# Kernel optimization log

Measured on AMD Instinct MI355X. Metric: run time of the kernel, lower is better.

Reference implementation:

```python
import jax, jax.numpy as jnp
import numpy as np

B, T, D, E, H = 4, 2048, 1024, 8, 4096

def setup_inputs() -> dict:
    key = jax.random.key(0)
    ks = jax.random.split(key, 10)
    s = 0.02
    return {
        "x": jax.random.normal(ks[0], (B, T, D), dtype=jnp.float32),
        "gate_w": jax.random.normal(ks[1], (D, E), dtype=jnp.float32) * s,
        "gate_b": jnp.zeros((E,), dtype=jnp.float32),
        "w1": jax.random.normal(ks[2], (E, D, H), dtype=jnp.float32) * s,
        "b1": jnp.zeros((E, H), dtype=jnp.float32),
        "w2": jax.random.normal(ks[3], (E, D, H), dtype=jnp.float32) * s,
        "b2": jnp.zeros((E, H), dtype=jnp.float32),
        "wp": jax.random.normal(ks[4], (E, H, D), dtype=jnp.float32) * s,
        "bp": jnp.zeros((E, D), dtype=jnp.float32),
        "k": 2,
    }

def reference(x, gate_w, gate_b, w1, b1, w2, b2, wp, bp, k):
    Bq, Tq, Dq = x.shape
    Eq = gate_w.shape[1]
    xf = x.reshape(-1, Dq)                          # [N, D]
    logits = xf @ gate_w + gate_b                   # [N, E]
    topk_scores, topk_idx = jax.lax.top_k(logits, k)  # [N, k]
    gate_probs = jax.nn.softmax(topk_scores, axis=-1)  # [N, k]
    onehot = jax.nn.one_hot(topk_idx, Eq, dtype=x.dtype)  # [N, k, E]
    # per-token per-expert combine weight (0 if expert not in top-k)
    combine = jnp.einsum('nk,nke->ne', gate_probs, onehot)  # [N, E]
    expert_counts = onehot.sum(axis=(0, 1))               # [E]
    out = jnp.zeros_like(xf)
    for e in range(Eq):  # small static loop over experts
        h = jax.nn.silu(xf @ w1[e] + b1[e]) * (xf @ w2[e] + b2[e])  # [N, H]
        y = h @ wp[e] + bp[e]                                       # [N, D]
        out = out + combine[:, e:e + 1] * y
    aux = jnp.sum((expert_counts / expert_counts.sum() - 1.0 / Eq) ** 2)
    return out.reshape(Bq, Tq, Dq), aux
```

## Files before the change

### kernel.cpp

```cpp
#include <hip/hip_runtime.h>
#include <cstdint>
#include <cstddef>

#define N_TOK 8192
#define DIM   1024
#define NEXP  8
#define HID   4096
#define WELEM 4194304ull

typedef __attribute__((ext_vector_type(8))) short short8v;
typedef __attribute__((ext_vector_type(4))) float f32x4;

__device__ __forceinline__ unsigned short f2bf(float f) {
  unsigned u = __builtin_bit_cast(unsigned, f);
  u += 0x7fffu + ((u >> 16) & 1u);
  return (unsigned short)(u >> 16);
}

__device__ __forceinline__ void gload16(const void* g, void* l) {
  __builtin_amdgcn_global_load_lds(
      (const __attribute__((address_space(1))) void*)g,
      (__attribute__((address_space(3))) void*)l, 16, 0, 0);
}

__global__ void convert_x_k(const float* __restrict__ x, unsigned short* __restrict__ xb) {
  size_t i = ((size_t)blockIdx.x * 256 + threadIdx.x) * 8;
  float4 a = *(const float4*)(x + i);
  float4 b = *(const float4*)(x + i + 4);
  short8v v;
  v[0] = (short)f2bf(a.x); v[1] = (short)f2bf(a.y); v[2] = (short)f2bf(a.z); v[3] = (short)f2bf(a.w);
  v[4] = (short)f2bf(b.x); v[5] = (short)f2bf(b.y); v[6] = (short)f2bf(b.z); v[7] = (short)f2bf(b.w);
  *(short8v*)(xb + i) = v;
}

__global__ void gate2_k(const float* __restrict__ x, const float* __restrict__ gw,
                        const float* __restrict__ gb, int* __restrict__ tassign,
                        float2* __restrict__ tprob) {
  int lane = threadIdx.x & 63, wid = threadIdx.x >> 6;
  int t = blockIdx.x * 4 + wid;
  const float* xr = x + (size_t)t * DIM;
  float acc[NEXP];
#pragma unroll
  for (int e = 0; e < NEXP; ++e) acc[e] = 0.f;
#pragma unroll
  for (int j = 0; j < DIM / 256; ++j) {
    int d0 = j * 256 + lane * 4;
    float4 xv = *(const float4*)(xr + d0);
    const float* gp = gw + (size_t)d0 * NEXP;
#pragma unroll
    for (int c = 0; c < 4; ++c) {
      float xs = (c == 0) ? xv.x : (c == 1) ? xv.y : (c == 2) ? xv.z : xv.w;
      float4 g0 = *(const float4*)(gp + c * NEXP);
      float4 g1 = *(const float4*)(gp + c * NEXP + 4);
      acc[0] += xs * g0.x; acc[1] += xs * g0.y; acc[2] += xs * g0.z; acc[3] += xs * g0.w;
      acc[4] += xs * g1.x; acc[5] += xs * g1.y; acc[6] += xs * g1.z; acc[7] += xs * g1.w;
    }
  }
#pragma unroll
  for (int e = 0; e < NEXP; ++e) {
    float v = acc[e];
#pragma unroll
    for (int s = 1; s < 64; s <<= 1) v += __shfl_xor(v, s);
    acc[e] = v;
  }
  if (lane == 0) {
    float lg[NEXP];
#pragma unroll
    for (int e = 0; e < NEXP; ++e) lg[e] = acc[e] + gb[e];
    int i0 = 0;
#pragma unroll
    for (int e = 1; e < NEXP; ++e) if (lg[e] > lg[i0]) i0 = e;
    int i1 = -1;
#pragma unroll
    for (int e = 0; e < NEXP; ++e) if (e != i0 && (i1 < 0 || lg[e] > lg[i1])) i1 = e;
    float ex = expf(lg[i1] - lg[i0]);
    float p0 = 1.f / (1.f + ex);
    float p1 = ex * p0;
    tassign[t] = i0 | (i1 << 8);
    tprob[t] = make_float2(p0, p1);
  }
}

__global__ void route_k(const int* __restrict__ tassign, const float2* __restrict__ tprob,
                        int* __restrict__ rtok, float* __restrict__ rwgt,
                        int* __restrict__ counts, int* __restrict__ ebase) {
  __shared__ int h[NEXP];
  __shared__ int cur[NEXP];
  int tid = threadIdx.x;
  if (tid < NEXP) h[tid] = 0;
  __syncthreads();
  for (int t = tid; t < N_TOK; t += 256) {
    int a = tassign[t];
    atomicAdd(&h[a & 255], 1);
    atomicAdd(&h[(a >> 8) & 255], 1);
  }
  __syncthreads();
  if (tid == 0) {
    int b = 0;
    for (int e = 0; e < NEXP; ++e) { counts[e] = h[e]; ebase[e] = b; cur[e] = b; b += h[e]; }
  }
  __syncthreads();
  for (int t = tid; t < N_TOK; t += 256) {
    int a = tassign[t];
    float2 p = tprob[t];
    int p0 = atomicAdd(&cur[a & 255], 1);
    rtok[p0] = t; rwgt[p0] = p.x;
    int p1 = atomicAdd(&cur[(a >> 8) & 255], 1);
    rtok[p1] = t; rwgt[p1] = p.y;
  }
}

__global__ void aux_k(const int* __restrict__ counts, float* __restrict__ out) {
  if (threadIdx.x == 0) {
    float tot = 0.f, c[NEXP];
    for (int e = 0; e < NEXP; ++e) { c[e] = (float)counts[e]; tot += c[e]; }
    float a = 0.f;
    for (int e = 0; e < NEXP; ++e) { float d = c[e] / tot - 0.125f; a += d * d; }
    out[(size_t)N_TOK * DIM] = a;
  }
}

__global__ void tcvt_k(const float* __restrict__ w1, const float* __restrict__ w2,
                       const float* __restrict__ wp, unsigned short* __restrict__ d1,
                       unsigned short* __restrict__ d2, unsigned short* __restrict__ d3) {
  int tile = blockIdx.x, mat = blockIdx.y;
  size_t eo = (size_t)blockIdx.z * WELEM;
  const float* src; unsigned short* dst; int R, C;
  if (mat == 0)      { src = w1 + eo; dst = d1 + eo; R = DIM; C = HID; }
  else if (mat == 1) { src = w2 + eo; dst = d2 + eo; R = DIM; C = HID; }
  else               { src = wp + eo; dst = d3 + eo; R = HID; C = DIM; }
  int tilesC = C >> 5;
  int tr = (tile / tilesC) << 5;
  int tc = (tile % tilesC) << 5;
  __shared__ float tl[32][33];
  int tx = threadIdx.x & 31, ty = threadIdx.x >> 5;
#pragma unroll
  for (int i = 0; i < 32; i += 8) tl[ty + i][tx] = src[(size_t)(tr + ty + i) * C + tc + tx];
  __syncthreads();
#pragma unroll
  for (int i = 0; i < 32; i += 8) dst[(size_t)(tc + ty + i) * R + tr + tx] = f2bf(tl[tx][ty + i]);
}

template<int DUMMY>
__global__ __launch_bounds__(256, 3) void gemm12m_k(
    const unsigned short* __restrict__ xb,
    const unsigned short* __restrict__ w1b, const unsigned short* __restrict__ w2b,
    const float* __restrict__ b1, const float* __restrict__ b2,
    const int* __restrict__ rtok, const int* __restrict__ counts,
    const int* __restrict__ ebase, const int* __restrict__ gbase,
    unsigned short* __restrict__ Gx, int e0) {
  int f = blockIdx.x + gridDim.x * (blockIdx.y + gridDim.y * blockIdx.z);
  int total = gridDim.x * gridDim.y * gridDim.z;
  int cpx = total >> 3;
  int nf = (f & 7) * cpx + (f >> 3);
  int pe = gridDim.x * gridDim.y;
  int ez = nf / pe;
  int r  = nf - ez * pe;
  int ntb = r >> 5;
  int mt  = r & 31;

  const int e = e0 + ez;
  const int ce = counts[e];
  if (mt * 128 >= ce) return;
  const int rb = ebase[e];
  const int gb_ = gbase[e];
  const unsigned short* w1t = w1b + (size_t)ez * WELEM;
  const unsigned short* w2t = w2b + (size_t)ez * WELEM;
  const float* b1e = b1 + (size_t)e * HID;
  const float* b2e = b2 + (size_t)e * HID;

  __shared__ __attribute__((aligned(16))) unsigned short sA[128 * 64];
  __shared__ __attribute__((aligned(16))) unsigned short sB1[64 * 64];
  __shared__ __attribute__((aligned(16))) unsigned short sB2[64 * 64];

  const int tid = threadIdx.x;
  const int lane = tid & 63, wid = tid >> 6;
  const int wm = wid >> 1, wn = wid & 1;
  const unsigned stg = (unsigned)(wid * 1024);

  const int grow = tid >> 3;
  const int lcol = ((tid & 7) ^ (grow & 7)) << 3;
  int sl0 = mt * 128 + grow;
  int c0 = sl0 < ce ? sl0 : ce - 1;
  int c1 = sl0 + 32 < ce ? sl0 + 32 : ce - 1;
  int c2 = sl0 + 64 < ce ? sl0 + 64 : ce - 1;
  int c3 = sl0 + 96 < ce ? sl0 + 96 : ce - 1;
  const unsigned short* pa0 = xb + (size_t)rtok[rb + c0] * DIM + lcol;
  const unsigned short* pa1 = xb + (size_t)rtok[rb + c1] * DIM + lcol;
  const unsigned short* pa2 = xb + (size_t)rtok[rb + c2] * DIM + lcol;
  const unsigned short* pa3 = xb + (size_t)rtok[rb + c3] * DIM + lcol;
  const unsigned short* pq1 = w1t + (size_t)(ntb * 64 + grow) * DIM + lcol;
  const unsigned short* pq2 = w2t + (size_t)(ntb * 64 + grow) * DIM + lcol;

  f32x4 acc1[4][2] = {};
  f32x4 acc2[4][2] = {};

#pragma unroll 1
  for (int t = 0; t < 16; ++t) {
    const int k0 = t * 64;
    __syncthreads();
    gload16(pa0 + k0, (char*)sA + stg);
    gload16(pa1 + k0, (char*)sA + stg + 4096);
    gload16(pa2 + k0, (char*)sA + stg + 8192);
    gload16(pa3 + k0, (char*)sA + stg + 12288);
    gload16(pq1 + k0, (char*)sB1 + stg);
    gload16(pq1 + k0 + 32 * DIM, (char*)sB1 + stg + 4096);
    gload16(pq2 + k0, (char*)sB2 + stg);
    gload16(pq2 + k0 + 32 * DIM, (char*)sB2 + stg + 4096);
    __syncthreads();
#pragma unroll
    for (int s = 0; s < 2; ++s) {
      short8v af[4], bf1[2], bf2[2];
#pragma unroll
      for (int m = 0; m < 4; ++m) {
        int row = wm * 64 + m * 16 + (lane & 15);
        int p = (s * 4 + (lane >> 4)) ^ (row & 7);
        af[m] = *(const short8v*)((const char*)sA + row * 128 + p * 16);
      }
#pragma unroll
      for (int n = 0; n < 2; ++n) {
        int row = wn * 32 + n * 16 + (lane & 15);
        int p = (s * 4 + (lane >> 4)) ^ (row & 7);
        bf1[n] = *(const short8v*)((const char*)sB1 + row * 128 + p * 16);
        bf2[n] = *(const short8v*)((const char*)sB2 + row * 128 + p * 16);
      }
#pragma unroll
      for (int m = 0; m < 4; ++m)
#pragma unroll
        for (int n = 0; n < 2; ++n) {
          acc1[m][n] = __builtin_amdgcn_mfma_f32_16x16x32_bf16(af[m], bf1[n], acc1[m][n], 0, 0, 0);
          acc2[m][n] = __builtin_amdgcn_mfma_f32_16x16x32_bf16(af[m], bf2[n], acc2[m][n], 0, 0, 0);
        }
    }
  }

#pragma unroll
  for (int n = 0; n < 2; ++n) {
    int col = ntb * 64 + wn * 32 + n * 16 + (lane & 15);
    float bb1 = b1e[col], bb2 = b2e[col];
#pragma unroll
    for (int m = 0; m < 4; ++m) {
      int rbase = mt * 128 + wm * 64 + m * 16 + ((lane >> 4) << 2);
#pragma unroll
      for (int r2 = 0; r2 < 4; ++r2) {
        int slot = rbase + r2;
        if (slot < ce) {
          float h1 = acc1[m][n][r2] + bb1;
          float h2 = acc2[m][n][r2] + bb2;
          float sg = 1.0f / (1.0f + __expf(-h1));
          Gx[(size_t)(gb_ + slot) * HID + col] = f2bf(h1 * sg * h2);
        }
      }
    }
  }
}

#define STG(SD, P0, P1, P2, P3, K0)                                 \
  gload16(P0 + (K0), (char*)SD + stg);                              \
  gload16(P1 + (K0), (char*)SD + stg + 4096);                       \
  gload16(P2 + (K0), (char*)SD + stg + 8192);                       \
  gload16(P3 + (K0), (char*)SD + stg + 12288);

#define CMP()                                                       \
  {                                                                 \
    _Pragma("unroll")                                               \
    for (int s = 0; s < 2; ++s) {                                   \
      short8v af[4], bf[4];                                         \
      _Pragma("unroll")                                             \
      for (int m = 0; m < 4; ++m) {                                 \
        int row = wm * 64 + m * 16 + (lane & 15);                   \
        int p = (s * 4 + (lane >> 4)) ^ (row & 7);                  \
        af[m] = *(const short8v*)((const char*)sA + row * 128 + p * 16); \
      }                                                             \
      _Pragma("unroll")                                             \
      for (int n = 0; n < 4; ++n) {                                 \
        int row = wn * 64 + n * 16 + (lane & 15);                   \
        int p = (s * 4 + (lane >> 4)) ^ (row & 7);                  \
        bf[n] = *(const short8v*)((const char*)sB + row * 128 + p * 16); \
      }                                                             \
      _Pragma("unroll")                                             \
      for (int m = 0; m < 4; ++m)                                   \
        _Pragma("unroll")                                           \
        for (int n = 0; n < 4; ++n)                                 \
          acc[m][n] = __builtin_amdgcn_mfma_f32_16x16x32_bf16(af[m], bf[n], acc[m][n], 0, 0, 0); \
    }                                                               \
  }

#define GEMM_LOOP(NTILE)                                            \
  _Pragma("unroll 1")                                               \
  for (int t = 0; t < (NTILE); ++t) {                               \
    __syncthreads();                                                \
    STG(sA, pa0, pa1, pa2, pa3, t * 64);                            \
    STG(sB, pb0, pb1, pb2, pb3, t * 64);                            \
    __syncthreads();                                                \
    CMP();                                                          \
  }

__global__ __launch_bounds__(256, 4) void gemm3n_k(
    const unsigned short* __restrict__ Gx, const unsigned short* __restrict__ wpb,
    const float* __restrict__ bp, const int* __restrict__ rtok,
    const float* __restrict__ rwgt, const int* __restrict__ counts,
    const int* __restrict__ ebase, const int* __restrict__ gbase,
    float* __restrict__ out, int e0) {
  int f = blockIdx.x + gridDim.x * (blockIdx.y + gridDim.y * blockIdx.z);
  int total = gridDim.x * gridDim.y * gridDim.z;
  int cpx = total >> 3;
  int nf = (f & 7) * cpx + (f >> 3);
  int pe = gridDim.x * gridDim.y;
  int ez = nf / pe;
  int r  = nf - ez * pe;
  int ntb = r >> 5;
  int mt  = r & 31;

  const int e = e0 + ez;
  const int ce = counts[e];
  if (mt * 128 >= ce) return;
  const int rb = ebase[e];
  const int gb_ = gbase[e];
  const unsigned short* wpt = wpb + (size_t)ez * WELEM;
  const float* bpe = bp + (size_t)e * DIM;

  __shared__ __attribute__((aligned(16))) unsigned short sA[128 * 64];
  __shared__ __attribute__((aligned(16))) unsigned short sB[128 * 64];

  const int tid = threadIdx.x;
  const int lane = tid & 63, wid = tid >> 6;
  const int wm = wid >> 1, wn = wid & 1;
  const unsigned stg = (unsigned)(wid * 1024);

  const int grow = tid >> 3;
  const int lcol = ((tid & 7) ^ (grow & 7)) << 3;
  int sl0 = mt * 128 + grow;
  int c0 = sl0 < ce ? sl0 : ce - 1;
  int c1 = sl0 + 32 < ce ? sl0 + 32 : ce - 1;
  int c2 = sl0 + 64 < ce ? sl0 + 64 : ce - 1;
  int c3 = sl0 + 96 < ce ? sl0 + 96 : ce - 1;
  const unsigned short* pa0 = Gx + (size_t)(gb_ + c0) * HID + lcol;
  const unsigned short* pa1 = Gx + (size_t)(gb_ + c1) * HID + lcol;
  const unsigned short* pa2 = Gx + (size_t)(gb_ + c2) * HID + lcol;
  const unsigned short* pa3 = Gx + (size_t)(gb_ + c3) * HID + lcol;
  const unsigned short* pb0 = wpt + (size_t)(ntb * 128 + grow) * HID + lcol;
  const unsigned short* pb1 = pb0 + (size_t)32 * HID;
  const unsigned short* pb2 = pb0 + (size_t)64 * HID;
  const unsigned short* pb3 = pb0 + (size_t)96 * HID;

  f32x4 acc[4][4] = {};
  GEMM_LOOP(64);

#pragma unroll
  for (int n = 0; n < 4; ++n) {
    int col = ntb * 128 + wn * 64 + n * 16 + (lane & 15);
    float bb = bpe[col];
#pragma unroll
    for (int m = 0; m < 4; ++m) {
      int rbase = mt * 128 + wm * 64 + m * 16 + ((lane >> 4) << 2);
#pragma unroll
      for (int r2 = 0; r2 < 4; ++r2) {
        int slot = rbase + r2;
        if (slot < ce) {
          int tok = rtok[rb + slot];
          float w = rwgt[rb + slot];
          atomicAdd(out + (size_t)tok * DIM + col, w * (acc[m][n][r2] + bb));
        }
      }
    }
  }
}

extern "C" void kernel_launch(void* const* d_in, const int* in_sizes, int n_in,
                              void* d_out, int out_size, void* d_ws, size_t ws_size,
                              hipStream_t stream) {
  const float* x  = (const float*)d_in[0];
  const float* gw = (const float*)d_in[1];
  const float* gb = (const float*)d_in[2];
  const float* w1 = (const float*)d_in[3];
  const float* b1 = (const float*)d_in[4];
  const float* w2 = (const float*)d_in[5];
  const float* b2 = (const float*)d_in[6];
  const float* wp = (const float*)d_in[7];
  const float* bp = (const float*)d_in[8];
  float* out = (float*)d_out;

  char* ws = (char*)d_ws;
  const size_t BIG_NEED = 352551008ull;
  bool big = ws_size >= BIG_NEED;

  unsigned short* xb = (unsigned short*)ws;
  unsigned short *Gp, *w1a, *w2a, *wpa;
  int* tassign; float2* tprob; int* rtok; float* rwgt; int* meta;
  if (big) {
    Gp  = (unsigned short*)(ws + 16777216);
    w1a = (unsigned short*)(ws + 150994944);
    w2a = (unsigned short*)(ws + 218103808);
    wpa = (unsigned short*)(ws + 285212672);
    tassign = (int*)(ws + 352321536);
    tprob   = (float2*)(ws + 352354304);
    rtok    = (int*)(ws + 352419840);
    rwgt    = (float*)(ws + 352485376);
    meta    = (int*)(ws + 352550912);
  } else {
    Gp  = (unsigned short*)(ws + 16777216);
    w1a = (unsigned short*)(ws + 83886080);
    w2a = (unsigned short*)(ws + 92274688);
    wpa = (unsigned short*)(ws + 100663296);
    tassign = (int*)(ws + 109051904);
    tprob   = (float2*)(ws + 109084672);
    rtok    = (int*)(ws + 109150208);
    rwgt    = (float*)(ws + 109215744);
    meta    = (int*)(ws + 109281280);
  }
  int* counts = meta;
  int* ebase  = meta + 8;
  int* zbase  = meta + 16;

  hipMemsetAsync(meta, 0, 96, stream);
  hipMemsetAsync(out, 0, (size_t)(N_TOK * DIM + 1) * sizeof(float), stream);

  convert_x_k<<<4096, 256, 0, stream>>>(x, xb);
  gate2_k<<<N_TOK / 4, 256, 0, stream>>>(x, gw, gb, tassign, tprob);
  route_k<<<1, 256, 0, stream>>>(tassign, tprob, rtok, rwgt, counts, ebase);
  aux_k<<<1, 64, 0, stream>>>(counts, out);

  if (big) {
    tcvt_k<<<dim3(4096, 3, NEXP), 256, 0, stream>>>(w1, w2, wp, w1a, w2a, wpa);
    gemm12m_k<0><<<dim3(32, 64, NEXP), 256, 0, stream>>>(
        xb, w1a, w2a, b1, b2, rtok, counts, ebase, ebase, Gp, 0);
    gemm3n_k<<<dim3(32, 8, NEXP), 256, 0, stream>>>(
        Gp, wpa, bp, rtok, rwgt, counts, ebase, ebase, out, 0);
  } else {
    for (int e = 0; e < NEXP; ++e) {
      tcvt_k<<<dim3(4096, 3, 1), 256, 0, stream>>>(
          w1 + (size_t)e * WELEM, w2 + (size_t)e * WELEM, wp + (size_t)e * WELEM,
          w1a, w2a, wpa);
      gemm12m_k<0><<<dim3(32, 64, 1), 256, 0, stream>>>(
          xb, w1a, w2a, b1, b2, rtok, counts, ebase, zbase, Gp, e);
      gemm3n_k<<<dim3(32, 8, 1), 256, 0, stream>>>(
          Gp, wpa, bp, rtok, rwgt, counts, ebase, zbase, out, e);
    }
  }
}
```

Measured before the change: 817.4 us.

## Double-buffer LDS tiles in both expert GEMMs to overlap loads with MFMA

Result: slower. 1.055 ms (+29.1%).

```diff
diff --git a/kernel.cpp b/kernel.cpp
--- a/kernel.cpp
+++ b/kernel.cpp
@@ -22,6 +22,13 @@
       (const __attribute__((address_space(1))) void*)g,
       (__attribute__((address_space(3))) void*)l, 16, 0, 0);
 }
+
+#define VMW8 do { asm volatile("s_waitcnt vmcnt(8)" ::: "memory"); \
+                  __builtin_amdgcn_sched_barrier(0); } while (0)
+#define VMW0 do { asm volatile("s_waitcnt vmcnt(0)" ::: "memory"); \
+                  __builtin_amdgcn_sched_barrier(0); } while (0)
+#define BARR do { __builtin_amdgcn_s_barrier(); \
+                  __builtin_amdgcn_sched_barrier(0); } while (0)
 
 __global__ void convert_x_k(const float* __restrict__ x, unsigned short* __restrict__ xb) {
   size_t i = ((size_t)blockIdx.x * 256 + threadIdx.x) * 8;
@@ -142,7 +149,7 @@
 }
 
 template<int DUMMY>
-__global__ __launch_bounds__(256, 3) void gemm12m_k(
+__global__ __launch_bounds__(256, 2) void gemm12m_k(
     const unsigned short* __restrict__ xb,
     const unsigned short* __restrict__ w1b, const unsigned short* __restrict__ w2b,
     const float* __restrict__ b1, const float* __restrict__ b2,
@@ -169,9 +176,9 @@
   const float* b1e = b1 + (size_t)e * HID;
   const float* b2e = b2 + (size_t)e * HID;
 
-  __shared__ __attribute__((aligned(16))) unsigned short sA[128 * 64];
-  __shared__ __attribute__((aligned(16))) unsigned short sB1[64 * 64];
-  __shared__ __attribute__((aligned(16))) unsigned short sB2[64 * 64];
+  __shared__ __attribute__((aligned(16))) unsigned short sA[2][128 * 64];
+  __shared__ __attribute__((aligned(16))) unsigned short sB1[2][64 * 64];
+  __shared__ __attribute__((aligned(16))) unsigned short sB2[2][64 * 64];
 
   const int tid = threadIdx.x;
   const int lane = tid & 63, wid = tid >> 6;
@@ -195,44 +202,63 @@
   f32x4 acc1[4][2] = {};
   f32x4 acc2[4][2] = {};
 
+#define STAGE12(BUF, K0)                                            \
+  gload16(pa0 + (K0), (char*)sA[BUF] + stg);                        \
+  gload16(pa1 + (K0), (char*)sA[BUF] + stg + 4096);                 \
+  gload16(pa2 + (K0), (char*)sA[BUF] + stg + 8192);                 \
+  gload16(pa3 + (K0), (char*)sA[BUF] + stg + 12288);                \
+  gload16(pq1 + (K0), (char*)sB1[BUF] + stg);                       \
+  gload16(pq1 + (K0) + 32 * DIM, (char*)sB1[BUF] + stg + 4096);     \
+  gload16(pq2 + (K0), (char*)sB2[BUF] + stg);                       \
+  gload16(pq2 + (K0) + 32 * DIM, (char*)sB2[BUF] + stg + 4096);
+
+#define CMP12(BUF)                                                  \
+  {                                                                 \
+    _Pragma("unroll")                                               \
+    for (int s = 0; s < 2; ++s) {                                   \
+      short8v af[4], bf1[2], bf2[2];                                \
+      _Pragma("unroll")                                             \
+      for (int m = 0; m < 4; ++m) {                                 \
+        int row = wm * 64 + m * 16 + (lane & 15);                   \
+        int p = (s * 4 + (lane >> 4)) ^ (row & 7);                  \
+        af[m] = *(const short8v*)((const char*)sA[BUF] + row * 128 + p * 16); \
+      }                                                             \
+      _Pragma("unroll")                                             \
+      for (int n = 0; n < 2; ++n) {                                 \
+        int row = wn * 32 + n * 16 + (lane & 15);                   \
+        int p = (s * 4 + (lane >> 4)) ^ (row & 7);                  \
+        bf1[n] = *(const short8v*)((const char*)sB1[BUF] + row * 128 + p * 16); \
+        bf2[n] = *(const short8v*)((const char*)sB2[BUF] + row * 128 + p * 16); \
+      }                                                             \
+      _Pragma("unroll")                                             \
+      for (int m = 0; m < 4; ++m)                                   \
+        _Pragma("unroll")                                           \
+        for (int n = 0; n < 2; ++n) {                               \
+          acc1[m][n] = __builtin_amdgcn_mfma_f32_16x16x32_bf16(af[m], bf1[n], acc1[m][n], 0, 0, 0); \
+          acc2[m][n] = __builtin_amdgcn_mfma_f32_16x16x32_bf16(af[m], bf2[n], acc2[m][n], 0, 0, 0); \
+        }                                                           \
+    }                                                               \
+  }
+
+  STAGE12(0, 0);
 #pragma unroll 1
-  for (int t = 0; t < 16; ++t) {
-    const int k0 = t * 64;
-    __syncthreads();
-    gload16(pa0 + k0, (char*)sA + stg);
-    gload16(pa1 + k0, (char*)sA + stg + 4096);
-    gload16(pa2 + k0, (char*)sA + stg + 8192);
-    gload16(pa3 + k0, (char*)sA + stg + 12288);
-    gload16(pq1 + k0, (char*)sB1 + stg);
-    gload16(pq1 + k0 + 32 * DIM, (char*)sB1 + stg + 4096);
-    gload16(pq2 + k0, (char*)sB2 + stg);
-    gload16(pq2 + k0 + 32 * DIM, (char*)sB2 + stg + 4096);
-    __syncthreads();
-#pragma unroll
-    for (int s = 0; s < 2; ++s) {
-      short8v af[4], bf1[2], bf2[2];
-#pragma unroll
-      for (int m = 0; m < 4; ++m) {
-        int row = wm * 64 + m * 16 + (lane & 15);
-        int p = (s * 4 + (lane >> 4)) ^ (row & 7);
-        af[m] = *(const short8v*)((const char*)sA + row * 128 + p * 16);
-      }
-#pragma unroll
-      for (int n = 0; n < 2; ++n) {
-        int row = wn * 32 + n * 16 + (lane & 15);
-        int p = (s * 4 + (lane >> 4)) ^ (row & 7);
-        bf1[n] = *(const short8v*)((const char*)sB1 + row * 128 + p * 16);
-        bf2[n] = *(const short8v*)((const char*)sB2 + row * 128 + p * 16);
-      }
-#pragma unroll
-      for (int m = 0; m < 4; ++m)
-#pragma unroll
-        for (int n = 0; n < 2; ++n) {
-          acc1[m][n] = __builtin_amdgcn_mfma_f32_16x16x32_bf16(af[m], bf1[n], acc1[m][n], 0, 0, 0);
-          acc2[m][n] = __builtin_amdgcn_mfma_f32_16x16x32_bf16(af[m], bf2[n], acc2[m][n], 0, 0, 0);
-        }
-    }
-  }
+  for (int i = 0; i < 7; ++i) {
+    STAGE12(1, (2 * i + 1) * 64);
+    VMW8; BARR;
+    CMP12(0);
+    BARR;
+    STAGE12(0, (2 * i + 2) * 64);
+    VMW8; BARR;
+    CMP12(1);
+    BARR;
+  }
+  STAGE12(1, 15 * 64);
+  VMW8; BARR;
+  CMP12(0);
+  VMW0; BARR;
+  CMP12(1);
+#undef STAGE12
+#undef CMP12
 
 #pragma unroll
   for (int n = 0; n < 2; ++n) {
@@ -255,48 +281,7 @@
   }
 }
 
-#define STG(SD, P0, P1, P2, P3, K0)                                 \
-  gload16(P0 + (K0), (char*)SD + stg);                              \
-  gload16(P1 + (K0), (char*)SD + stg + 4096);                       \
-  gload16(P2 + (K0), (char*)SD + stg + 8192);                       \
-  gload16(P3 + (K0), (char*)SD + stg + 12288);
-
-#define CMP()                                                       \
-  {                                                                 \
-    _Pragma("unroll")                                               \
-    for (int s = 0; s < 2; ++s) {                                   \
-      short8v af[4], bf[4];                                         \
-      _Pragma("unroll")                                             \
-      for (int m = 0; m < 4; ++m) {                                 \
-        int row = wm * 64 + m * 16 + (lane & 15);                   \
-        int p = (s * 4 + (lane >> 4)) ^ (row & 7);                  \
-        af[m] = *(const short8v*)((const char*)sA + row * 128 + p * 16); \
-      }                                                             \
-      _Pragma("unroll")                                             \
-      for (int n = 0; n < 4; ++n) {                                 \
-        int row = wn * 64 + n * 16 + (lane & 15);                   \
-        int p = (s * 4 + (lane >> 4)) ^ (row & 7);                  \
-        bf[n] = *(const short8v*)((const char*)sB + row * 128 + p * 16); \
-      }                                                             \
-      _Pragma("unroll")                                             \
-      for (int m = 0; m < 4; ++m)                                   \
-        _Pragma("unroll")                                           \
-        for (int n = 0; n < 4; ++n)                                 \
-          acc[m][n] = __builtin_amdgcn_mfma_f32_16x16x32_bf16(af[m], bf[n], acc[m][n], 0, 0, 0); \
-    }                                                               \
-  }
-
-#define GEMM_LOOP(NTILE)                                            \
-  _Pragma("unroll 1")                                               \
-  for (int t = 0; t < (NTILE); ++t) {                               \
-    __syncthreads();                                                \
-    STG(sA, pa0, pa1, pa2, pa3, t * 64);                            \
-    STG(sB, pb0, pb1, pb2, pb3, t * 64);                            \
-    __syncthreads();                                                \
-    CMP();                                                          \
-  }
-
-__global__ __launch_bounds__(256, 4) void gemm3n_k(
+__global__ __launch_bounds__(256, 2) void gemm3n_k(
     const unsigned short* __restrict__ Gx, const unsigned short* __restrict__ wpb,
     const float* __restrict__ bp, const int* __restrict__ rtok,
     const float* __restrict__ rwgt, const int* __restrict__ counts,
@@ -320,8 +305,8 @@
   const unsigned short* wpt = wpb + (size_t)ez * WELEM;
   const float* bpe = bp + (size_t)e * DIM;
 
-  __shared__ __attribute__((aligned(16))) unsigned short sA[128 * 64];
-  __shared__ __attribute__((aligned(16))) unsigned short sB[128 * 64];
+  __shared__ __attribute__((aligned(16))) unsigned short sA[2][128 * 64];
+  __shared__ __attribute__((aligned(16))) unsigned short sB[2][128 * 64];
 
   const int tid = threadIdx.x;
   const int lane = tid & 63, wid = tid >> 6;
@@ -345,7 +330,61 @@
   const unsigned short* pb3 = pb0 + (size_t)96 * HID;
 
   f32x4 acc[4][4] = {};
-  GEMM_LOOP(64);
+
+#define STG3(BUF, K0)                                               \
+  gload16(pa0 + (K0), (char*)sA[BUF] + stg);                        \
+  gload16(pa1 + (K0), (char*)sA[BUF] + stg + 4096);                 \
+  gload16(pa2 + (K0), (char*)sA[BUF] + stg + 8192);                 \
+  gload16(pa3 + (K0), (char*)sA[BUF] + stg + 12288);                \
+  gload16(pb0 + (K0), (char*)sB[BUF] + stg);                        \
+  gload16(pb1 + (K0), (char*)sB[BUF] + stg + 4096);                 \
+  gload16(pb2 + (K0), (char*)sB[BUF] + stg + 8192);                 \
+  gload16(pb3 + (K0), (char*)sB[BUF] + stg + 12288);
+
+#define CMP3(BUF)                                                   \
+  {                                                                 \
+    _Pragma("unroll")                                               \
+    for (int s = 0; s < 2; ++s) {                                   \
+      short8v af[4], bf[4];                                         \
+      _Pragma("unroll")                                             \
+      for (int m = 0; m < 4; ++m) {                                 \
+        int row = wm * 64 + m * 16 + (lane & 15);                   \
+        int p = (s * 4 + (lane >> 4)) ^ (row & 7);                  \
+        af[m] = *(const short8v*)((const char*)sA[BUF] + row * 128 + p * 16); \
+      }                                                             \
+      _Pragma("unroll")                                             \
+      for (int n = 0; n < 4; ++n) {                                 \
+        int row = wn * 64 + n * 16 + (lane & 15);                   \
+        int p = (s * 4 + (lane >> 4)) ^ (row & 7);                  \
+        bf[n] = *(const short8v*)((const char*)sB[BUF] + row * 128 + p * 16); \
+      }                                                             \
+      _Pragma("unroll")                                             \
+      for (int m = 0; m < 4; ++m)                                   \
+        _Pragma("unroll")                                           \
+        for (int n = 0; n < 4; ++n)                                 \
+          acc[m][n] = __builtin_amdgcn_mfma_f32_16x16x32_bf16(af[m], bf[n], acc[m][n], 0, 0, 0); \
+    }                                                               \
+  }
+
+  STG3(0, 0);
+#pragma unroll 1
+  for (int i = 0; i < 31; ++i) {
+    STG3(1, (2 * i + 1) * 64);
+    VMW8; BARR;
+    CMP3(0);
+    BARR;
+    STG3(0, (2 * i + 2) * 64);
+    VMW8; BARR;
+    CMP3(1);
+    BARR;
+  }
+  STG3(1, 63 * 64);
+  VMW8; BARR;
+  CMP3(0);
+  VMW0; BARR;
+  CMP3(1);
+#undef STG3
+#undef CMP3
 
 #pragma unroll
   for (int n = 0; n < 4; ++n) {
```

## Fuse x bf16 conversion into gate, vectorize weight transpose, raise gemm occupancy

Applied to the files above, without the earlier changes.

Result: no change. 805.6 us (-1.4%).

```diff
diff --git a/kernel.cpp b/kernel.cpp
--- a/kernel.cpp
+++ b/kernel.cpp
@@ -9,6 +9,8 @@
 #define WELEM 4194304ull
 
 typedef __attribute__((ext_vector_type(8))) short short8v;
+typedef __attribute__((ext_vector_type(8))) unsigned short ushort8v;
+typedef __attribute__((ext_vector_type(4))) unsigned short ushort4v;
 typedef __attribute__((ext_vector_type(4))) float f32x4;
 
 __device__ __forceinline__ unsigned short f2bf(float f) {
@@ -23,22 +25,13 @@
       (__attribute__((address_space(3))) void*)l, 16, 0, 0);
 }
 
-__global__ void convert_x_k(const float* __restrict__ x, unsigned short* __restrict__ xb) {
-  size_t i = ((size_t)blockIdx.x * 256 + threadIdx.x) * 8;
-  float4 a = *(const float4*)(x + i);
-  float4 b = *(const float4*)(x + i + 4);
-  short8v v;
-  v[0] = (short)f2bf(a.x); v[1] = (short)f2bf(a.y); v[2] = (short)f2bf(a.z); v[3] = (short)f2bf(a.w);
-  v[4] = (short)f2bf(b.x); v[5] = (short)f2bf(b.y); v[6] = (short)f2bf(b.z); v[7] = (short)f2bf(b.w);
-  *(short8v*)(xb + i) = v;
-}
-
 __global__ void gate2_k(const float* __restrict__ x, const float* __restrict__ gw,
                         const float* __restrict__ gb, int* __restrict__ tassign,
-                        float2* __restrict__ tprob) {
+                        float2* __restrict__ tprob, unsigned short* __restrict__ xb) {
   int lane = threadIdx.x & 63, wid = threadIdx.x >> 6;
   int t = blockIdx.x * 4 + wid;
   const float* xr = x + (size_t)t * DIM;
+  unsigned short* xbr = xb + (size_t)t * DIM;
   float acc[NEXP];
 #pragma unroll
   for (int e = 0; e < NEXP; ++e) acc[e] = 0.f;
@@ -46,6 +39,9 @@
   for (int j = 0; j < DIM / 256; ++j) {
     int d0 = j * 256 + lane * 4;
     float4 xv = *(const float4*)(xr + d0);
+    ushort4v o;
+    o[0] = f2bf(xv.x); o[1] = f2bf(xv.y); o[2] = f2bf(xv.z); o[3] = f2bf(xv.w);
+    *(ushort4v*)(xbr + d0) = o;
     const float* gp = gw + (size_t)d0 * NEXP;
 #pragma unroll
     for (int c = 0; c < 4; ++c) {
@@ -129,20 +125,36 @@
   if (mat == 0)      { src = w1 + eo; dst = d1 + eo; R = DIM; C = HID; }
   else if (mat == 1) { src = w2 + eo; dst = d2 + eo; R = DIM; C = HID; }
   else               { src = wp + eo; dst = d3 + eo; R = HID; C = DIM; }
-  int tilesC = C >> 5;
-  int tr = (tile / tilesC) << 5;
-  int tc = (tile % tilesC) << 5;
-  __shared__ float tl[32][33];
-  int tx = threadIdx.x & 31, ty = threadIdx.x >> 5;
-#pragma unroll
-  for (int i = 0; i < 32; i += 8) tl[ty + i][tx] = src[(size_t)(tr + ty + i) * C + tc + tx];
+  int tilesC = C >> 6;
+  int tr = (tile / tilesC) << 6;
+  int tc = (tile % tilesC) << 6;
+  __shared__ float tl[64][65];
+  int tid = threadIdx.x;
+  int lr = tid >> 4;
+  int lc = (tid & 15) << 2;
+#pragma unroll
+  for (int i = 0; i < 4; ++i) {
+    float4 v = *(const float4*)(src + (size_t)(tr + lr + i * 16) * C + tc + lc);
+    tl[lr + i * 16][lc]     = v.x;
+    tl[lr + i * 16][lc + 1] = v.y;
+    tl[lr + i * 16][lc + 2] = v.z;
+    tl[lr + i * 16][lc + 3] = v.w;
+  }
   __syncthreads();
-#pragma unroll
-  for (int i = 0; i < 32; i += 8) dst[(size_t)(tc + ty + i) * R + tr + tx] = f2bf(tl[tx][ty + i]);
+  int oc = tid >> 3;
+  int orr = (tid & 7) << 3;
+#pragma unroll
+  for (int i = 0; i < 2; ++i) {
+    int c = oc + i * 32;
+    ushort8v v;
+#pragma unroll
+    for (int k = 0; k < 8; ++k) v[k] = f2bf(tl[orr + k][c]);
+    *(ushort8v*)(dst + (size_t)(tc + c) * R + tr + orr) = v;
+  }
 }
 
 template<int DUMMY>
-__global__ __launch_bounds__(256, 3) void gemm12m_k(
+__global__ __launch_bounds__(256, 4) void gemm12m_k(
     const unsigned short* __restrict__ xb,
     const unsigned short* __restrict__ w1b, const unsigned short* __restrict__ w2b,
     const float* __restrict__ b1, const float* __restrict__ b2,
@@ -416,20 +428,19 @@
   hipMemsetAsync(meta, 0, 96, stream);
   hipMemsetAsync(out, 0, (size_t)(N_TOK * DIM + 1) * sizeof(float), stream);
 
-  convert_x_k<<<4096, 256, 0, stream>>>(x, xb);
-  gate2_k<<<N_TOK / 4, 256, 0, stream>>>(x, gw, gb, tassign, tprob);
+  gate2_k<<<N_TOK / 4, 256, 0, stream>>>(x, gw, gb, tassign, tprob, xb);
   route_k<<<1, 256, 0, stream>>>(tassign, tprob, rtok, rwgt, counts, ebase);
   aux_k<<<1, 64, 0, stream>>>(counts, out);
 
   if (big) {
-    tcvt_k<<<dim3(4096, 3, NEXP), 256, 0, stream>>>(w1, w2, wp, w1a, w2a, wpa);
+    tcvt_k<<<dim3(1024, 3, NEXP), 256, 0, stream>>>(w1, w2, wp, w1a, w2a, wpa);
     gemm12m_k<0><<<dim3(32, 64, NEXP), 256, 0, stream>>>(
         xb, w1a, w2a, b1, b2, rtok, counts, ebase, ebase, Gp, 0);
     gemm3n_k<<<dim3(32, 8, NEXP), 256, 0, stream>>>(
         Gp, wpa, bp, rtok, rwgt, counts, ebase, ebase, out, 0);
   } else {
     for (int e = 0; e < NEXP; ++e) {
-      tcvt_k<<<dim3(4096, 3, 1), 256, 0, stream>>>(
+      tcvt_k<<<dim3(1024, 3, 1), 256, 0, stream>>>(
           w1 + (size_t)e * WELEM, w2 + (size_t)e * WELEM, wp + (size_t)e * WELEM,
           w1a, w2a, wpa);
       gemm12m_k<0><<<dim3(32, 64, 1), 256, 0, stream>>>(
```
